# Kernel tuning notes

Hardware: AMD Instinct MI355X
Metric: run time of the kernel (lower is better)

Reference implementation:

```python
import jax, jax.numpy as jnp
import numpy as np

B, C, H, W = 32, 512, 32, 32
N_WORDS, WORD_DIM = 77, 256
HW2 = H * W


def setup_inputs() -> dict:
    key = jax.random.key(0)
    k1, k2, k3 = jax.random.split(key, 3)
    feat = jax.random.normal(k1, (B, C, H, W), dtype=jnp.float32)
    word_emb = jax.random.normal(k2, (B, N_WORDS, WORD_DIM), dtype=jnp.float32)
    # nn.Linear(word_dim, img_hw*img_hw): weight (out,in), bias (out,)
    W_fc = jax.random.normal(k3, (HW2, WORD_DIM), dtype=jnp.float32) * (1.0 / np.sqrt(WORD_DIM))
    b_fc = jnp.zeros((HW2,), dtype=jnp.float32)
    return {"feat": feat, "word_emb": word_emb, "W_fc": W_fc, "b_fc": b_fc}


def reference(feat, word_emb, W_fc, b_fc):
    b, c, h, w = feat.shape
    f = feat.reshape(b, c, h * w)                                   # (b, c, hw2)
    we = jnp.einsum('bnd,kd->bnk', word_emb, W_fc) + b_fc           # (b, n, hw2)
    we = jnp.swapaxes(we, 1, 2)                                     # (b, hw2, n)
    scores = jnp.einsum('bck,bkn->bcn', f, we)                      # (b, c, n)
    att = jax.nn.softmax(scores, axis=-1)                           # (b, c, n)
    att_feat = jnp.einsum('bcn,bkn->bck', att, we)                  # (b, c, hw2)
    return att_feat.reshape(b, c, h, w)
```

## Files before the change

### kernel.cpp

```cpp
#include <hip/hip_runtime.h>

#define B_    32
#define C_    512
#define HW2_  1024
#define NW    77
#define NP    80
#define NPT   96
#define WD    256

typedef unsigned int   uint32;
typedef unsigned short u16;
typedef __attribute__((ext_vector_type(8))) short bf16x8;
typedef __attribute__((ext_vector_type(4))) float f32x4;

#define MFMA(a, b, c) __builtin_amdgcn_mfma_f32_16x16x32_bf16(a, b, c, 0, 0, 0)

#define WE_ELN   ((size_t)B_ * NP * HW2_ / 8)
#define WET_ELN  ((size_t)B_ * HW2_ * NPT / 8)
#define W_ELN    ((size_t)HW2_ * WD / 8)
#define E_ELN    ((size_t)B_ * NP * WD / 8)

__device__ __forceinline__ void split1(float x, u16 &h, u16 &l) {
    uint32 u = __float_as_uint(x);
    h = (u16)(u >> 16);
    float r = x - __uint_as_float(u & 0xffff0000u);
    uint32 v = __float_as_uint(r);
    l = (u16)((v + 0x7fffu + ((v >> 16) & 1u)) >> 16);
}

__device__ __forceinline__ void split8(float4 a, float4 b, bf16x8 &h, bf16x8 &l) {
    float v[8] = {a.x, a.y, a.z, a.w, b.x, b.y, b.z, b.w};
    #pragma unroll
    for (int i = 0; i < 8; ++i) {
        u16 hh, ll; split1(v[i], hh, ll);
        h[i] = (short)hh; l[i] = (short)ll;
    }
}

__global__ __launch_bounds__(256) void split_pre(
    const float* __restrict__ W_fc, const float* __restrict__ word_emb,
    bf16x8* __restrict__ Wh, bf16x8* __restrict__ Wl,
    bf16x8* __restrict__ Eh, bf16x8* __restrict__ El)
{
    const int g = blockIdx.x * 256 + threadIdx.x;
    if (g < (int)W_ELN) {
        float4 x = *(const float4*)(W_fc + g * 8);
        float4 y = *(const float4*)(W_fc + g * 8 + 4);
        bf16x8 h, l; split8(x, y, h, l);
        Wh[g] = h; Wl[g] = l;
    } else {
        const int e = g - (int)W_ELN;
        const int b = e / 2560, r = e % 2560;
        const int n = r >> 5, gg = r & 31;
        bf16x8 h = (bf16x8)(short)0, l = h;
        if (n < NW) {
            const float* p = word_emb + ((size_t)(b * NW + n)) * WD + gg * 8;
            float4 x = *(const float4*)p, y = *(const float4*)(p + 4);
            split8(x, y, h, l);
        }
        Eh[e] = h; El[e] = l;
    }
}

__global__ __launch_bounds__(256, 2) void we_gemm(
    const bf16x8* __restrict__ Wh, const bf16x8* __restrict__ Wl,
    const bf16x8* __restrict__ Eh, const bf16x8* __restrict__ El,
    const float* __restrict__ b_fc,
    bf16x8* __restrict__ we_hi, bf16x8* __restrict__ we_lo,
    bf16x8* __restrict__ weT_hi, bf16x8* __restrict__ weT_lo)
{
    __shared__ __align__(16) uint32 HL[NP][68];

    const int id = blockIdx.x;
    const int b  = (id & 7) + 8 * (id >> 7);
    const int kb = ((id >> 3) & 15) * 64;
    const int t  = threadIdx.x;
    const int w  = t >> 6, lane = t & 63, lr = lane & 15, lg = lane >> 4;
    const int kout = kb + 16 * w + lr;

    f32x4 acc[5];
    #pragma unroll
    for (int m = 0; m < 5; ++m) acc[m] = (f32x4)0.0f;

    const bf16x8* wrh = Wh + kout * 32;
    const bf16x8* wrl = Wl + kout * 32;
    const bf16x8* ebh = Eh + (b * NP + lr) * 32;
    const bf16x8* ebl = El + (b * NP + lr) * 32;

    #pragma unroll
    for (int ks = 0; ks < 8; ++ks) {
        const int o = ks * 4 + lg;
        const bf16x8 bh = wrh[o], bl = wrl[o];
        #pragma unroll
        for (int m = 0; m < 5; ++m) {
            const bf16x8 ah = ebh[m * 512 + o];
            const bf16x8 al = ebl[m * 512 + o];
            acc[m] = MFMA(ah, bh, acc[m]);
            acc[m] = MFMA(ah, bl, acc[m]);
            acc[m] = MFMA(al, bh, acc[m]);
            acc[m] = MFMA(al, bl, acc[m]);
        }
    }

    const float bias = b_fc[kout];
    #pragma unroll
    for (int m = 0; m < 5; ++m)
        #pragma unroll
        for (int r = 0; r < 4; ++r) {
            u16 hh, ll; split1(acc[m][r] + bias, hh, ll);
            HL[16 * m + 4 * lg + r][16 * w + lr] = ((uint32)hh << 16) | ll;
        }
    __syncthreads();

    #pragma unroll
    for (int u0 = 0; u0 < 640; u0 += 256) {
        const int u = u0 + t;
        if (u < 640) {
            const int n = u >> 3, c8 = (u & 7) * 8;
            uint4 p0 = *(const uint4*)&HL[n][c8];
            uint4 p1 = *(const uint4*)&HL[n][c8 + 4];
            const uint32 pw[8] = {p0.x, p0.y, p0.z, p0.w, p1.x, p1.y, p1.z, p1.w};
            bf16x8 hv, lv;
            #pragma unroll
            for (int i = 0; i < 8; ++i) {
                hv[i] = (short)(pw[i] >> 16);
                lv[i] = (short)(pw[i] & 0xffffu);
            }
            const int o = ((b * NP + n) * HW2_ + kb + c8) >> 3;
            we_hi[o] = hv; we_lo[o] = lv;
        }
    }
    if (t < 128) {
        const int kr = t & 63, sel = t >> 6;
        bf16x8* dst = (sel ? weT_lo : weT_hi) + (((b * HW2_ + kb + kr) * NPT) >> 3);
        #pragma unroll
        for (int g = 0; g < 12; ++g) {
            bf16x8 v;
            #pragma unroll
            for (int i = 0; i < 8; ++i) {
                const int n = g * 8 + i;
                const uint32 p = (n < NP) ? HL[n][kr] : 0u;
                v[i] = (short)(sel ? (p & 0xffffu) : (p >> 16));
            }
            dst[g] = v;
        }
    }
}

__global__ __launch_bounds__(256, 3) void attn_mfma(
    const float* __restrict__ feat,
    const bf16x8* __restrict__ we_hi, const bf16x8* __restrict__ we_lo,
    const bf16x8* __restrict__ weT_hi, const bf16x8* __restrict__ weT_lo,
    float* __restrict__ out)
{
    __shared__ __align__(16) float S[4][16][84];
    __shared__ __align__(16) u16   Ph[16][NPT];
    __shared__ __align__(16) u16   Pl[16][NPT];

    const int id  = blockIdx.x;
    const int b   = (id & 7) + 8 * (id >> 8);
    const int c0  = ((id >> 3) & 31) * 16;

    const int t    = threadIdx.x;
    const int h    = t >> 6;
    const int lane = t & 63, lr = lane & 15, lg = lane >> 4;

    f32x4 acc[5];
    #pragma unroll
    for (int m = 0; m < 5; ++m) acc[m] = (f32x4)0.0f;

    const float*  frow = feat + (size_t)(b * C_ + c0 + lr) * HW2_;
    const bf16x8* wh   = we_hi + (size_t)b * (NP * HW2_ / 8);
    const bf16x8* wl   = we_lo + (size_t)b * (NP * HW2_ / 8);

    float4 fx[2], fy[2];
    bf16x8 AH[2][5], AL[2][5];

#define P1_LOAD(slot, ksv) do {                                   \
        const int kk_ = h * 256 + (ksv) * 32 + 8 * lg;            \
        fx[slot] = *(const float4*)(frow + kk_);                  \
        fy[slot] = *(const float4*)(frow + kk_ + 4);              \
        const int go_ = h * 32 + (ksv) * 4 + lg;                  \
        _Pragma("unroll")                                         \
        for (int m_ = 0; m_ < 5; ++m_) {                          \
            AH[slot][m_] = wh[(16 * m_ + lr) * 128 + go_];        \
            AL[slot][m_] = wl[(16 * m_ + lr) * 128 + go_];        \
        } } while (0)

    P1_LOAD(0, 0);
    #pragma unroll
    for (int ks = 0; ks < 8; ++ks) {
        if (ks < 7) {
            if ((ks & 1) == 0) P1_LOAD(1, ks + 1);
            else               P1_LOAD(0, ks + 1);
        }
        const int cur = ks & 1;
        bf16x8 fh, fl; split8(fx[cur], fy[cur], fh, fl);
        #pragma unroll
        for (int m = 0; m < 5; ++m) {
            acc[m] = MFMA(AH[cur][m], fh, acc[m]);
            acc[m] = MFMA(AH[cur][m], fl, acc[m]);
            acc[m] = MFMA(AL[cur][m], fh, acc[m]);
        }
    }
#undef P1_LOAD

    #pragma unroll
    for (int m = 0; m < 5; ++m)
        #pragma unroll
        for (int r = 0; r < 4; ++r)
            S[h][lr][16 * m + 4 * lg + r] = acc[m][r];
    __syncthreads();

    {
        const int srow = 4 * h + (lane >> 4), scol = lane & 15;
        float v5[6];
        float mx = -3.0e38f;
        #pragma unroll
        for (int j = 0; j < 6; ++j) {
            const int n = scol + 16 * j;
            float sv = 0.f;
            if (j < 5) {
                sv = S[0][srow][n] + S[1][srow][n] + S[2][srow][n] + S[3][srow][n];
                if (n < NW) mx = fmaxf(mx, sv);
            }
            v5[j] = sv;
        }
        mx = fmaxf(mx, __shfl_xor(mx, 1));
        mx = fmaxf(mx, __shfl_xor(mx, 2));
        mx = fmaxf(mx, __shfl_xor(mx, 4));
        mx = fmaxf(mx, __shfl_xor(mx, 8));
        float sum = 0.f;
        #pragma unroll
        for (int j = 0; j < 6; ++j) {
            const int n = scol + 16 * j;
            const float e = (n < NW) ? __expf(v5[j] - mx) : 0.f;
            v5[j] = e; sum += e;
        }
        sum += __shfl_xor(sum, 1);
        sum += __shfl_xor(sum, 2);
        sum += __shfl_xor(sum, 4);
        sum += __shfl_xor(sum, 8);
        const float inv = 1.0f / sum;
        #pragma unroll
        for (int j = 0; j < 6; ++j) {
            const int n = scol + 16 * j;
            u16 ph, pl; split1(v5[j] * inv, ph, pl);
            Ph[srow][n] = ph; Pl[srow][n] = pl;
        }
    }
    __syncthreads();

    bf16x8 pbh[3], pbl[3];
    #pragma unroll
    for (int ksn = 0; ksn < 3; ++ksn) {
        pbh[ksn] = *(const bf16x8*)&Ph[lr][32 * ksn + 8 * lg];
        pbl[ksn] = *(const bf16x8*)&Pl[lr][32 * ksn + 8 * lg];
    }
    const bf16x8* th = weT_hi + (size_t)b * (HW2_ * NPT / 8);
    const bf16x8* tl = weT_lo + (size_t)b * (HW2_ * NPT / 8);
    float* orow = out + (size_t)(b * C_ + c0 + lr) * HW2_;

    bf16x8 WA[3], WB[3];

#define P3_LOAD(slot, g) do {                                     \
        const int ci_ = (g) / 12, s_ = (g) % 12;                  \
        const int kt_ = s_ & 3, ksn_ = s_ >> 2;                   \
        const int row_ = (ci_ * 4 + h) * 64 + 16 * kt_ + lr;      \
        const int off_ = row_ * 12 + 4 * ksn_ + lg;               \
        WA[slot] = th[off_]; WB[slot] = tl[off_]; } while (0)

    P3_LOAD(0, 0);
    P3_LOAD(1, 1);
    #pragma unroll
    for (int ci = 0; ci < 4; ++ci) {
        f32x4 o[4];
        #pragma unroll
        for (int kt = 0; kt < 4; ++kt) o[kt] = (f32x4)0.0f;
        #pragma unroll
        for (int s = 0; s < 12; ++s) {
            const int g = ci * 12 + s;
            if (g < 46) {
                const int sl = (g + 2) % 3;
                if (sl == 0)      P3_LOAD(0, g + 2);
                else if (sl == 1) P3_LOAD(1, g + 2);
                else              P3_LOAD(2, g + 2);
            }
            const int cs = g % 3, kt = s & 3, ksn = s >> 2;
            o[kt] = MFMA(WA[cs], pbh[ksn], o[kt]);
            o[kt] = MFMA(WA[cs], pbl[ksn], o[kt]);
            o[kt] = MFMA(WB[cs], pbh[ksn], o[kt]);
        }
        const int kb2 = (ci * 4 + h) * 64;
        #pragma unroll
        for (int kt = 0; kt < 4; ++kt) {
            float4 v = make_float4(o[kt][0], o[kt][1], o[kt][2], o[kt][3]);
            *(float4*)(orow + kb2 + 16 * kt + 4 * lg) = v;
        }
    }
#undef P3_LOAD
}

extern "C" void kernel_launch(void* const* d_in, const int* in_sizes, int n_in,
                              void* d_out, int out_size, void* d_ws, size_t ws_size,
                              hipStream_t stream) {
    (void)in_sizes; (void)n_in; (void)out_size; (void)ws_size;
    const float* feat     = (const float*)d_in[0];
    const float* word_emb = (const float*)d_in[1];
    const float* W_fc     = (const float*)d_in[2];
    const float* b_fc     = (const float*)d_in[3];

    bf16x8* we_hi  = (bf16x8*)d_ws;
    bf16x8* we_lo  = we_hi  + WE_ELN;
    bf16x8* weT_hi = we_lo  + WE_ELN;
    bf16x8* weT_lo = weT_hi + WET_ELN;
    bf16x8* Wh     = weT_lo + WET_ELN;
    bf16x8* Wl     = Wh + W_ELN;
    bf16x8* Eh     = Wl + W_ELN;
    bf16x8* El     = Eh + E_ELN;

    split_pre<<<448, 256, 0, stream>>>(W_fc, word_emb, Wh, Wl, Eh, El);
    we_gemm<<<512, 256, 0, stream>>>(Wh, Wl, Eh, El, b_fc, we_hi, we_lo, weT_hi, weT_lo);
    attn_mfma<<<1024, 256, 0, stream>>>(feat, we_hi, we_lo, weT_hi, weT_lo, (float*)d_out);
}
```

Before: 212.9 us.

## Process 32 channels per block and tile we layout for reuse

The attention kernel now handles two 16-channel groups per block, so each loaded we/weT fragment feeds twice as many MFMAs and the grid is halved. The we buffer is stored in a k-block-tiled layout so phase-one loads are contiguous, and the weT transpose write is spread across all 256 threads instead of 128. Explicit software prefetch double-buffering is removed in favour of straight-line loads, and occupancy hints change, which may expose more load latency and raise register pressure.

```diff
diff --git a/kernel.cpp b/kernel.cpp
--- a/kernel.cpp
+++ b/kernel.cpp
@@ -15,10 +15,10 @@
 
 #define MFMA(a, b, c) __builtin_amdgcn_mfma_f32_16x16x32_bf16(a, b, c, 0, 0, 0)
 
-#define WE_ELN   ((size_t)B_ * NP * HW2_ / 8)
-#define WET_ELN  ((size_t)B_ * HW2_ * NPT / 8)
-#define W_ELN    ((size_t)HW2_ * WD / 8)
-#define E_ELN    ((size_t)B_ * NP * WD / 8)
+#define WE_ELN   ((size_t)B_ * 16 * NP * 8)
+#define WET_ELN  ((size_t)B_ * HW2_ * 12)
+#define W_ELN    ((size_t)HW2_ * 32)
+#define E_ELN    ((size_t)B_ * NP * 32)
 
 __device__ __forceinline__ void split1(float x, u16 &h, u16 &l) {
     uint32 u = __float_as_uint(x);
@@ -62,7 +62,7 @@
     }
 }
 
-__global__ __launch_bounds__(256, 2) void we_gemm(
+__global__ __launch_bounds__(256) void we_gemm(
     const bf16x8* __restrict__ Wh, const bf16x8* __restrict__ Wl,
     const bf16x8* __restrict__ Eh, const bf16x8* __restrict__ El,
     const float* __restrict__ b_fc,
@@ -73,7 +73,8 @@
 
     const int id = blockIdx.x;
     const int b  = (id & 7) + 8 * (id >> 7);
-    const int kb = ((id >> 3) & 15) * 64;
+    const int q  = (id >> 3) & 15;
+    const int kb = q * 64;
     const int t  = threadIdx.x;
     const int w  = t >> 6, lane = t & 63, lr = lane & 15, lg = lane >> 4;
     const int kout = kb + 16 * w + lr;
@@ -126,179 +127,164 @@
                 hv[i] = (short)(pw[i] >> 16);
                 lv[i] = (short)(pw[i] & 0xffffu);
             }
-            const int o = ((b * NP + n) * HW2_ + kb + c8) >> 3;
+            const int o = ((b * 16 + q) * NP + n) * 8 + (u & 7);
             we_hi[o] = hv; we_lo[o] = lv;
         }
     }
-    if (t < 128) {
-        const int kr = t & 63, sel = t >> 6;
-        bf16x8* dst = (sel ? weT_lo : weT_hi) + (((b * HW2_ + kb + kr) * NPT) >> 3);
-        #pragma unroll
-        for (int g = 0; g < 12; ++g) {
-            bf16x8 v;
-            #pragma unroll
-            for (int i = 0; i < 8; ++i) {
-                const int n = g * 8 + i;
-                const uint32 p = (n < NP) ? HL[n][kr] : 0u;
-                v[i] = (short)(sel ? (p & 0xffffu) : (p >> 16));
-            }
-            dst[g] = v;
-        }
-    }
-}
-
-__global__ __launch_bounds__(256, 3) void attn_mfma(
+    #pragma unroll
+    for (int v0 = 0; v0 < 1536; v0 += 256) {
+        const int v = v0 + t;
+        const int sel = v >= 768;
+        const int r2  = sel ? v - 768 : v;
+        const int row = r2 / 12, g = r2 % 12;
+        bf16x8 val;
+        #pragma unroll
+        for (int i = 0; i < 8; ++i) {
+            const int n = g * 8 + i;
+            const uint32 p = (n < NP) ? HL[n][row] : 0u;
+            val[i] = (short)(sel ? (p & 0xffffu) : (p >> 16));
+        }
+        (sel ? weT_lo : weT_hi)[(b * HW2_ + kb + row) * 12 + g] = val;
+    }
+}
+
+__global__ __launch_bounds__(256, 2) void attn_mfma(
     const float* __restrict__ feat,
     const bf16x8* __restrict__ we_hi, const bf16x8* __restrict__ we_lo,
     const bf16x8* __restrict__ weT_hi, const bf16x8* __restrict__ weT_lo,
     float* __restrict__ out)
 {
     __shared__ __align__(16) float S[4][16][84];
-    __shared__ __align__(16) u16   Ph[16][NPT];
-    __shared__ __align__(16) u16   Pl[16][NPT];
+    __shared__ __align__(16) u16   Ph[32][NPT];
+    __shared__ __align__(16) u16   Pl[32][NPT];
 
     const int id  = blockIdx.x;
-    const int b   = (id & 7) + 8 * (id >> 8);
-    const int c0  = ((id >> 3) & 31) * 16;
+    const int b   = (id & 7) + 8 * (id >> 7);
+    const int c0  = ((id >> 3) & 15) * 32;
 
     const int t    = threadIdx.x;
     const int h    = t >> 6;
     const int lane = t & 63, lr = lane & 15, lg = lane >> 4;
 
-    f32x4 acc[5];
-    #pragma unroll
-    for (int m = 0; m < 5; ++m) acc[m] = (f32x4)0.0f;
-
-    const float*  frow = feat + (size_t)(b * C_ + c0 + lr) * HW2_;
-    const bf16x8* wh   = we_hi + (size_t)b * (NP * HW2_ / 8);
-    const bf16x8* wl   = we_lo + (size_t)b * (NP * HW2_ / 8);
-
-    float4 fx[2], fy[2];
-    bf16x8 AH[2][5], AL[2][5];
-
-#define P1_LOAD(slot, ksv) do {                                   \
-        const int kk_ = h * 256 + (ksv) * 32 + 8 * lg;            \
-        fx[slot] = *(const float4*)(frow + kk_);                  \
-        fy[slot] = *(const float4*)(frow + kk_ + 4);              \
-        const int go_ = h * 32 + (ksv) * 4 + lg;                  \
-        _Pragma("unroll")                                         \
-        for (int m_ = 0; m_ < 5; ++m_) {                          \
-            AH[slot][m_] = wh[(16 * m_ + lr) * 128 + go_];        \
-            AL[slot][m_] = wl[(16 * m_ + lr) * 128 + go_];        \
-        } } while (0)
-
-    P1_LOAD(0, 0);
+    f32x4 acc[2][5];
+    #pragma unroll
+    for (int s = 0; s < 2; ++s)
+        #pragma unroll
+        for (int m = 0; m < 5; ++m) acc[s][m] = (f32x4)0.0f;
+
+    const float* frow0 = feat + (size_t)(b * C_ + c0 + lr) * HW2_;
+    const float* frow1 = frow0 + 16 * HW2_;
+
     #pragma unroll
     for (int ks = 0; ks < 8; ++ks) {
-        if (ks < 7) {
-            if ((ks & 1) == 0) P1_LOAD(1, ks + 1);
-            else               P1_LOAD(0, ks + 1);
-        }
-        const int cur = ks & 1;
-        bf16x8 fh, fl; split8(fx[cur], fy[cur], fh, fl);
+        const int kk = h * 256 + ks * 32 + 8 * lg;
+        bf16x8 fh0, fl0, fh1, fl1;
+        {   float4 x = *(const float4*)(frow0 + kk);
+            float4 y = *(const float4*)(frow0 + kk + 4);
+            split8(x, y, fh0, fl0); }
+        {   float4 x = *(const float4*)(frow1 + kk);
+            float4 y = *(const float4*)(frow1 + kk + 4);
+            split8(x, y, fh1, fl1); }
+        const int qb  = (b * 16 + h * 4 + (ks >> 1)) * NP;
+        const int sub = (ks & 1) * 4 + lg;
         #pragma unroll
         for (int m = 0; m < 5; ++m) {
-            acc[m] = MFMA(AH[cur][m], fh, acc[m]);
-            acc[m] = MFMA(AH[cur][m], fl, acc[m]);
-            acc[m] = MFMA(AL[cur][m], fh, acc[m]);
-        }
-    }
-#undef P1_LOAD
-
-    #pragma unroll
-    for (int m = 0; m < 5; ++m)
-        #pragma unroll
-        for (int r = 0; r < 4; ++r)
-            S[h][lr][16 * m + 4 * lg + r] = acc[m][r];
-    __syncthreads();
-
-    {
-        const int srow = 4 * h + (lane >> 4), scol = lane & 15;
-        float v5[6];
-        float mx = -3.0e38f;
-        #pragma unroll
-        for (int j = 0; j < 6; ++j) {
-            const int n = scol + 16 * j;
-            float sv = 0.f;
-            if (j < 5) {
-                sv = S[0][srow][n] + S[1][srow][n] + S[2][srow][n] + S[3][srow][n];
-                if (n < NW) mx = fmaxf(mx, sv);
+            const int o = (qb + 16 * m + lr) * 8 + sub;
+            const bf16x8 ah = we_hi[o];
+            const bf16x8 al = we_lo[o];
+            acc[0][m] = MFMA(ah, fh0, acc[0][m]);
+            acc[0][m] = MFMA(ah, fl0, acc[0][m]);
+            acc[0][m] = MFMA(al, fh0, acc[0][m]);
+            acc[1][m] = MFMA(ah, fh1, acc[1][m]);
+            acc[1][m] = MFMA(ah, fl1, acc[1][m]);
+            acc[1][m] = MFMA(al, fh1, acc[1][m]);
+        }
+    }
+
+    #pragma unroll
+    for (int s = 0; s < 2; ++s) {
+        #pragma unroll
+        for (int m = 0; m < 5; ++m)
+            #pragma unroll
+            for (int r = 0; r < 4; ++r)
+                S[h][lr][16 * m + 4 * lg + r] = acc[s][m][r];
+        __syncthreads();
+        {
+            const int srow = 4 * h + (lane >> 4), scol = lane & 15;
+            float v5[6];
+            float mx = -3.0e38f;
+            #pragma unroll
+            for (int j = 0; j < 6; ++j) {
+                const int n = scol + 16 * j;
+                float sv = 0.f;
+                if (j < 5) {
+                    sv = S[0][srow][n] + S[1][srow][n] + S[2][srow][n] + S[3][srow][n];
+                    if (n < NW) mx = fmaxf(mx, sv);
+                }
+                v5[j] = sv;
             }
-            v5[j] = sv;
-        }
-        mx = fmaxf(mx, __shfl_xor(mx, 1));
-        mx = fmaxf(mx, __shfl_xor(mx, 2));
-        mx = fmaxf(mx, __shfl_xor(mx, 4));
-        mx = fmaxf(mx, __shfl_xor(mx, 8));
-        float sum = 0.f;
-        #pragma unroll
-        for (int j = 0; j < 6; ++j) {
-            const int n = scol + 16 * j;
-            const float e = (n < NW) ? __expf(v5[j] - mx) : 0.f;
-            v5[j] = e; sum += e;
-        }
-        sum += __shfl_xor(sum, 1);
-        sum += __shfl_xor(sum, 2);
-        sum += __shfl_xor(sum, 4);
-        sum += __shfl_xor(sum, 8);
-        const float inv = 1.0f / sum;
-        #pragma unroll
-        for (int j = 0; j < 6; ++j) {
-            const int n = scol + 16 * j;
-            u16 ph, pl; split1(v5[j] * inv, ph, pl);
-            Ph[srow][n] = ph; Pl[srow][n] = pl;
-        }
-    }
-    __syncthreads();
-
-    bf16x8 pbh[3], pbl[3];
-    #pragma unroll
-    for (int ksn = 0; ksn < 3; ++ksn) {
-        pbh[ksn] = *(const bf16x8*)&Ph[lr][32 * ksn + 8 * lg];
-        pbl[ksn] = *(const bf16x8*)&Pl[lr][32 * ksn + 8 * lg];
-    }
-    const bf16x8* th = weT_hi + (size_t)b * (HW2_ * NPT / 8);
-    const bf16x8* tl = weT_lo + (size_t)b * (HW2_ * NPT / 8);
-    float* orow = out + (size_t)(b * C_ + c0 + lr) * HW2_;
-
-    bf16x8 WA[3], WB[3];
-
-#define P3_LOAD(slot, g) do {                                     \
-        const int ci_ = (g) / 12, s_ = (g) % 12;                  \
-        const int kt_ = s_ & 3, ksn_ = s_ >> 2;                   \
-        const int row_ = (ci_ * 4 + h) * 64 + 16 * kt_ + lr;      \
-        const int off_ = row_ * 12 + 4 * ksn_ + lg;               \
-        WA[slot] = th[off_]; WB[slot] = tl[off_]; } while (0)
-
-    P3_LOAD(0, 0);
-    P3_LOAD(1, 1);
-    #pragma unroll
-    for (int ci = 0; ci < 4; ++ci) {
-        f32x4 o[4];
-        #pragma unroll
-        for (int kt = 0; kt < 4; ++kt) o[kt] = (f32x4)0.0f;
-        #pragma unroll
-        for (int s = 0; s < 12; ++s) {
-            const int g = ci * 12 + s;
-            if (g < 46) {
-                const int sl = (g + 2) % 3;
-                if (sl == 0)      P3_LOAD(0, g + 2);
-                else if (sl == 1) P3_LOAD(1, g + 2);
-                else              P3_LOAD(2, g + 2);
+            mx = fmaxf(mx, __shfl_xor(mx, 1));
+            mx = fmaxf(mx, __shfl_xor(mx, 2));
+            mx = fmaxf(mx, __shfl_xor(mx, 4));
+            mx = fmaxf(mx, __shfl_xor(mx, 8));
+            float sum = 0.f;
+            #pragma unroll
+            for (int j = 0; j < 6; ++j) {
+                const int n = scol + 16 * j;
+                const float e = (n < NW) ? __expf(v5[j] - mx) : 0.f;
+                v5[j] = e; sum += e;
             }
-            const int cs = g % 3, kt = s & 3, ksn = s >> 2;
-            o[kt] = MFMA(WA[cs], pbh[ksn], o[kt]);
-            o[kt] = MFMA(WA[cs], pbl[ksn], o[kt]);
-            o[kt] = MFMA(WB[cs], pbh[ksn], o[kt]);
-        }
-        const int kb2 = (ci * 4 + h) * 64;
-        #pragma unroll
-        for (int kt = 0; kt < 4; ++kt) {
-            float4 v = make_float4(o[kt][0], o[kt][1], o[kt][2], o[kt][3]);
-            *(float4*)(orow + kb2 + 16 * kt + 4 * lg) = v;
-        }
-    }
-#undef P3_LOAD
+            sum += __shfl_xor(sum, 1);
+            sum += __shfl_xor(sum, 2);
+            sum += __shfl_xor(sum, 4);
+            sum += __shfl_xor(sum, 8);
+            const float inv = 1.0f / sum;
+            #pragma unroll
+            for (int j = 0; j < 6; ++j) {
+                const int n = scol + 16 * j;
+                u16 ph, pl; split1(v5[j] * inv, ph, pl);
+                Ph[16 * s + srow][n] = ph; Pl[16 * s + srow][n] = pl;
+            }
+        }
+        __syncthreads();
+    }
+
+    bf16x8 pbh[2][3], pbl[2][3];
+    #pragma unroll
+    for (int s = 0; s < 2; ++s)
+        #pragma unroll
+        for (int ksn = 0; ksn < 3; ++ksn) {
+            pbh[s][ksn] = *(const bf16x8*)&Ph[16 * s + lr][32 * ksn + 8 * lg];
+            pbl[s][ksn] = *(const bf16x8*)&Pl[16 * s + lr][32 * ksn + 8 * lg];
+        }
+    const bf16x8* th = weT_hi + (size_t)b * HW2_ * 12;
+    const bf16x8* tl = weT_lo + (size_t)b * HW2_ * 12;
+    float* orow0 = out + (size_t)(b * C_ + c0 + lr) * HW2_;
+    float* orow1 = orow0 + 16 * HW2_;
+
+    #pragma unroll
+    for (int tt = 0; tt < 16; ++tt) {
+        const int row = h * 256 + tt * 16 + lr;
+        bf16x8 wa[3], wb[3];
+        #pragma unroll
+        for (int ksn = 0; ksn < 3; ++ksn) {
+            wa[ksn] = th[row * 12 + 4 * ksn + lg];
+            wb[ksn] = tl[row * 12 + 4 * ksn + lg];
+        }
+        f32x4 o0 = (f32x4)0.0f, o1 = (f32x4)0.0f;
+        #pragma unroll
+        for (int ksn = 0; ksn < 3; ++ksn) {
+            o0 = MFMA(wa[ksn], pbh[0][ksn], o0);
+            o0 = MFMA(wa[ksn], pbl[0][ksn], o0);
+            o0 = MFMA(wb[ksn], pbh[0][ksn], o0);
+            o1 = MFMA(wa[ksn], pbh[1][ksn], o1);
+            o1 = MFMA(wa[ksn], pbl[1][ksn], o1);
+            o1 = MFMA(wb[ksn], pbh[1][ksn], o1);
+        }
+        const int col = h * 256 + tt * 16 + 4 * lg;
+        *(float4*)(orow0 + col) = make_float4(o0[0], o0[1], o0[2], o0[3]);
+        *(float4*)(orow1 + col) = make_float4(o1[0], o1[1], o1[2], o1[3]);
+    }
 }
 
 extern "C" void kernel_launch(void* const* d_in, const int* in_sizes, int n_in,
@@ -321,5 +307,5 @@
 
     split_pre<<<448, 256, 0, stream>>>(W_fc, word_emb, Wh, Wl, Eh, El);
     we_gemm<<<512, 256, 0, stream>>>(Wh, Wl, Eh, El, b_fc, we_hi, we_lo, weT_hi, weT_lo);
-    attn_mfma<<<1024, 256, 0, stream>>>(feat, we_hi, we_lo, weT_hi, weT_lo, (float*)d_out);
-}
+    attn_mfma<<<512, 256, 0, stream>>>(feat, we_hi, we_lo, weT_hi, weT_lo, (float*)d_out);
+}
```

Result: faster. 182.1 us (-14.4%).
